# Optimization experiments

Measured on AMD Instinct MI355X. Metric: run time of the kernel, lower is better.

## Reference

```python
import jax, jax.numpy as jnp
import numpy as np

# ---- fixed structuring elements (buffers, not trainable) ----
N_SCALES = 4
BASE = 2.0
ZERO_SCALE = 1.0
PAD_VAL = 10000.0

_scales = ZERO_SCALE ** 2 * np.power(BASE, np.arange(N_SCALES)) ** 2  # t_k = 4^k
_widths = [4 * int(np.ceil(np.sqrt(s))) for s in _scales]             # 4,8,16,32
SES = [jnp.asarray([(1.0 / (4.0 * t)) * x ** 2 for x in range(-w, w + 1)],
                   dtype=jnp.float32)
       for t, w in zip(_scales, _widths)]  # SE lengths 9,17,33,65 (all odd)


def _pool1d(im, se, c, axis, is_max):
    """Weighted sliding max/min along `axis` (separable morphological op).
    out[p] = max_j padded[p+j] - c*se[j]  (dilation) or min_j padded[p+j] + c*se[j]."""
    n = se.shape[0]
    w = n // 2  # n is odd -> symmetric pad, matches torch pad1==pad2
    pad_val = -PAD_VAL if is_max else PAD_VAL
    cfg = [(0, 0)] * im.ndim
    cfg[axis] = (w, w)
    padded = jnp.pad(im, cfg, constant_values=pad_val)
    L = im.shape[axis]

    def take(j):
        return jax.lax.dynamic_slice_in_dim(padded, j, L, axis)

    win = jax.vmap(take)(jnp.arange(n))          # [n, B, C, H, W]
    se_b = se.reshape((n,) + (1,) * im.ndim)     # broadcast over image dims
    if is_max:
        return jnp.max(win - c * se_b, axis=0)
    return jnp.min(win + c * se_b, axis=0)


def _sep_dilation(im, se, c):
    tmp = _pool1d(im, se, c, axis=-1, is_max=True)   # horizontal
    return _pool1d(tmp, se, c, axis=-2, is_max=True)  # vertical


def _sep_erosion(im, se, c):
    tmp = _pool1d(im, se, c, axis=-1, is_max=False)
    return _pool1d(tmp, se, c, axis=-2, is_max=False)


def setup_inputs() -> dict:
    key = jax.random.key(0)
    k1, _ = jax.random.split(key)
    inputs = jax.random.normal(k1, (4, 8, 256, 256), dtype=jnp.float32)
    se_coef = jnp.float32(0.5)
    return {"inputs": inputs, "se_coef": se_coef}


def reference(inputs, se_coef):
    # closing = erosion(dilation(x)) per scale, stacked on new axis 2
    outs = [_sep_erosion(_sep_dilation(inputs, se, se_coef), se, se_coef)
            for se in SES]
    return jnp.stack(outs, axis=2)  # [B, C, n_scales, H, W]
```

## Files before the change

### kernel.cpp

```cpp
#include <hip/hip_runtime.h>


#define HH 256
#define WW 256
#define BC 32
#define NS 4
#define HW (HH * WW)
#define SLICE ((long)BC * HW)
#define LSTR 324

template <int W, bool IS_MAX>
__device__ __forceinline__ void hpass_lds(const float* __restrict__ lw, float cw,
                                          float acc[8])
{
    const float PAD = IS_MAX ? -1e30f : 1e30f;
#pragma unroll
    for (int pp = 0; pp < 8; ++pp) acc[pp] = PAD;
#pragma unroll
    for (int u = 0; u < (8 + 2 * W) / 4; ++u) {
        const float4 vv = *(const float4*)(lw + 4 * u);
        const float vs[4] = {vv.x, vv.y, vv.z, vv.w};
#pragma unroll
        for (int pp = 0; pp < 8; ++pp) {
#pragma unroll
            for (int e = 0; e < 4; ++e) {
                const int d = 4 * u + e - W - pp;
                if (d >= -W && d <= W) {
                    const float K = (float)(d * d);
                    const float cand = IS_MAX ? fmaf(cw, -K, vs[e])
                                              : fmaf(cw,  K, vs[e]);
                    acc[pp] = IS_MAX ? fmaxf(acc[pp], cand) : fminf(acc[pp], cand);
                }
            }
        }
    }
}

template <int W, bool IS_MAX, bool CLAMP>
__device__ __forceinline__ void vpass_core(const float* __restrict__ img, int x,
                                           int h0, float cw, float acc[8])
{
    const float PAD = IS_MAX ? -1e30f : 1e30f;
#pragma unroll
    for (int pp = 0; pp < 8; ++pp) acc[pp] = PAD;
#pragma unroll
    for (int ch = 0; ch < (8 + 2 * W) / 8; ++ch) {
        float v[8];
#pragma unroll
        for (int q = 0; q < 8; ++q) {
            const int h = h0 + ch * 8 + q - W;
            if (CLAMP) {
                const int hc = min(max(h, 0), HH - 1);
                const float tv = img[(long)hc * WW + x];
                v[q] = (h == hc) ? tv : PAD;
            } else {
                v[q] = img[(long)h * WW + x];
            }
        }
#pragma unroll
        for (int pp = 0; pp < 8; ++pp) {
#pragma unroll
            for (int q = 0; q < 8; ++q) {
                const int d = ch * 8 + q - W - pp;
                if (d >= -W && d <= W) {
                    const float K = (float)(d * d);
                    const float cand = IS_MAX ? fmaf(cw, -K, v[q])
                                              : fmaf(cw,  K, v[q]);
                    acc[pp] = IS_MAX ? fmaxf(acc[pp], cand) : fminf(acc[pp], cand);
                }
            }
        }
    }
}

template <int W, bool IS_MAX>
__device__ __forceinline__ void vh_impl(const float* __restrict__ img,
                                        float* __restrict__ op_base,
                                        int h0, float c, float* lbuf)
{
    const int x = threadIdx.x;
    const float cw = c * (4.0f / (float)(W * W));
    const float PAD = IS_MAX ? -1e30f : 1e30f;

    float vacc[8];
    if (h0 >= W && h0 + 8 + W <= HH)
        vpass_core<W, IS_MAX, false>(img, x, h0, cw, vacc);
    else
        vpass_core<W, IS_MAX, true >(img, x, h0, cw, vacc);

#pragma unroll
    for (int q = 0; q < 8; ++q) lbuf[q * LSTR + W + x] = vacc[q];
    if (x < W) {
#pragma unroll
        for (int q = 0; q < 8; ++q) {
            lbuf[q * LSTR + x] = PAD;
            lbuf[q * LSTR + W + 256 + x] = PAD;
        }
    }
    __syncthreads();

    const int r = threadIdx.x >> 5, t = threadIdx.x & 31;
    float acc[8];
    hpass_lds<W, IS_MAX>(lbuf + r * LSTR + 8 * t, cw, acc);
    float* op = op_base + (long)(h0 + r) * WW + 8 * t;
    *(float4*)(op)     = make_float4(acc[0], acc[1], acc[2], acc[3]);
    *(float4*)(op + 4) = make_float4(acc[4], acc[5], acc[6], acc[7]);
}

template <bool IS_MAX>
__global__ __launch_bounds__(256, 8) void k_vh(const float* __restrict__ in,
                                               float* __restrict__ out,
                                               const float* __restrict__ cptr,
                                               long in_ks, long in_zs,
                                               long out_ks, long out_zs,
                                               int kbase, int kbits,
                                               int zbase, int zbits)
{
    __shared__ float lbuf[8 * LSTR];
    const int bid = blockIdx.x;
    const int k = kbase + (bid & ((1 << kbits) - 1));
    const int rest = bid >> kbits;
    const int z = zbase + (rest & ((1 << zbits) - 1));
    const int y = rest >> zbits;
    const int h0 = y * 8;
    const float c = cptr[0];
    const float* ip = in + (long)k * in_ks + (long)z * in_zs;
    float* op = out + (long)k * out_ks + (long)z * out_zs;
    switch (k) {
        case 0: vh_impl<4,  IS_MAX>(ip, op, h0, c, lbuf); break;
        case 1: vh_impl<8,  IS_MAX>(ip, op, h0, c, lbuf); break;
        case 2: vh_impl<16, IS_MAX>(ip, op, h0, c, lbuf); break;
        case 3: vh_impl<32, IS_MAX>(ip, op, h0, c, lbuf); break;
    }
}

extern "C" void kernel_launch(void* const* d_in, const int* in_sizes, int n_in,
                              void* d_out, int out_size, void* d_ws, size_t ws_size,
                              hipStream_t stream)
{
    const float* x = (const float*)d_in[0];
    const float* c = (const float*)d_in[1];
    float* out = (float*)d_out;
    float* ws  = (float*)d_ws;

    dim3 b(256);
    const size_t slice_b = (size_t)SLICE * sizeof(float);
    if (ws_size >= (size_t)NS * slice_b) {
        dim3 g(NS * BC * (HH / 8));
        k_vh<true ><<<g, b, 0, stream>>>(x,  ws,  c, 0,     HW, SLICE, HW,
                                         0, 2, 0, 5);
        k_vh<false><<<g, b, 0, stream>>>(ws, out, c, SLICE, HW, HW, (long)NS * HW,
                                         0, 2, 0, 5);
    } else if (ws_size >= slice_b) {
        dim3 g(BC * (HH / 8));
        for (int k = 0; k < NS; ++k) {
            k_vh<true ><<<g, b, 0, stream>>>(x,  ws,  c, 0, HW, 0, HW,
                                             k, 0, 0, 5);
            k_vh<false><<<g, b, 0, stream>>>(ws, out, c, 0, HW, HW, (long)NS * HW,
                                             k, 0, 0, 5);
        }
    } else {
        dim3 g(HH / 8);
        for (int k = 0; k < NS; ++k)
            for (int z = 0; z < BC; ++z) {
                k_vh<true ><<<g, b, 0, stream>>>(x,  ws,  c, 0, HW, 0, 0,
                                                 k, 0, z, 0);
                k_vh<false><<<g, b, 0, stream>>>(ws, out, c, 0, 0, HW, (long)NS * HW,
                                                 k, 0, z, 0);
            }
    }
}
```

Measured before the change: 133.0 us.

## Balance block work across scales by looping multiple row tiles for small windows

Blocks now process a variable number of 8-row tiles: scale 3 (widest window) gets one tile per block, while smaller scales loop over 2, 4 or 8 tiles. The grid shrinks from 128 to 60 blocks per slice, so per-block work is more even across scales and fewer light blocks are launched. A trailing barrier is added so LDS can be reused between tiles. In exchange there is less total parallelism, with 1920 blocks, and the small-scale blocks run their tiles serially.

New measurement: 119.7 us (median of 2 runs). 10.0% less time.

```diff
diff --git a/kernel.cpp b/kernel.cpp
--- a/kernel.cpp
+++ b/kernel.cpp
@@ -74,12 +74,11 @@
 }
 
 template <int W, bool IS_MAX>
-__device__ __forceinline__ void vh_impl(const float* __restrict__ img,
+__device__ __forceinline__ void vh_tile(const float* __restrict__ img,
                                         float* __restrict__ op_base,
-                                        int h0, float c, float* lbuf)
+                                        int h0, float cw, float* lbuf)
 {
     const int x = threadIdx.x;
-    const float cw = c * (4.0f / (float)(W * W));
     const float PAD = IS_MAX ? -1e30f : 1e30f;
 
     float vacc[8];
@@ -105,6 +104,19 @@
     float* op = op_base + (long)(h0 + r) * WW + 8 * t;
     *(float4*)(op)     = make_float4(acc[0], acc[1], acc[2], acc[3]);
     *(float4*)(op + 4) = make_float4(acc[4], acc[5], acc[6], acc[7]);
+
+    __syncthreads();
+}
+
+template <int W, bool IS_MAX, int NT>
+__device__ __forceinline__ void run_tiles(const float* __restrict__ ip,
+                                          float* __restrict__ op,
+                                          int y0, float c, float* lbuf)
+{
+    const float cw = c * (4.0f / (float)(W * W));
+#pragma unroll 1
+    for (int i = 0; i < NT; ++i)
+        vh_tile<W, IS_MAX>(ip, op, (y0 + i) * 8, cw, lbuf);
 }
 
 template <bool IS_MAX>
@@ -113,24 +125,33 @@
                                                const float* __restrict__ cptr,
                                                long in_ks, long in_zs,
                                                long out_ks, long out_zs,
-                                               int kbase, int kbits,
-                                               int zbase, int zbits)
+                                               int kfix, int bpz, int zbase)
 {
     __shared__ float lbuf[8 * LSTR];
     const int bid = blockIdx.x;
-    const int k = kbase + (bid & ((1 << kbits) - 1));
-    const int rest = bid >> kbits;
-    const int z = zbase + (rest & ((1 << zbits) - 1));
-    const int y = rest >> zbits;
-    const int h0 = y * 8;
+    int k, y0, z;
+    if (kfix < 0) {
+        z = bid / 60;
+        const int r = bid - z * 60;
+        if (r < 32)      { k = 3; y0 = r; }
+        else if (r < 48) { k = 2; y0 = (r - 32) * 2; }
+        else if (r < 56) { k = 1; y0 = (r - 48) * 4; }
+        else             { k = 0; y0 = (r - 56) * 8; }
+    } else {
+        k = kfix;
+        const int zi = bid / bpz;
+        const int yi = bid - zi * bpz;
+        z = zbase + zi;
+        y0 = yi * (32 / bpz);
+    }
     const float c = cptr[0];
     const float* ip = in + (long)k * in_ks + (long)z * in_zs;
     float* op = out + (long)k * out_ks + (long)z * out_zs;
     switch (k) {
-        case 0: vh_impl<4,  IS_MAX>(ip, op, h0, c, lbuf); break;
-        case 1: vh_impl<8,  IS_MAX>(ip, op, h0, c, lbuf); break;
-        case 2: vh_impl<16, IS_MAX>(ip, op, h0, c, lbuf); break;
-        case 3: vh_impl<32, IS_MAX>(ip, op, h0, c, lbuf); break;
+        case 0: run_tiles<4,  IS_MAX, 8>(ip, op, y0, c, lbuf); break;
+        case 1: run_tiles<8,  IS_MAX, 4>(ip, op, y0, c, lbuf); break;
+        case 2: run_tiles<16, IS_MAX, 2>(ip, op, y0, c, lbuf); break;
+        case 3: run_tiles<32, IS_MAX, 1>(ip, op, y0, c, lbuf); break;
     }
 }
 
@@ -146,27 +167,30 @@
     dim3 b(256);
     const size_t slice_b = (size_t)SLICE * sizeof(float);
     if (ws_size >= (size_t)NS * slice_b) {
-        dim3 g(NS * BC * (HH / 8));
+        dim3 g(60 * BC);
         k_vh<true ><<<g, b, 0, stream>>>(x,  ws,  c, 0,     HW, SLICE, HW,
-                                         0, 2, 0, 5);
+                                         -1, 0, 0);
         k_vh<false><<<g, b, 0, stream>>>(ws, out, c, SLICE, HW, HW, (long)NS * HW,
-                                         0, 2, 0, 5);
+                                         -1, 0, 0);
     } else if (ws_size >= slice_b) {
-        dim3 g(BC * (HH / 8));
         for (int k = 0; k < NS; ++k) {
+            const int bpz = 4 << k;
+            dim3 g(bpz * BC);
             k_vh<true ><<<g, b, 0, stream>>>(x,  ws,  c, 0, HW, 0, HW,
-                                             k, 0, 0, 5);
+                                             k, bpz, 0);
             k_vh<false><<<g, b, 0, stream>>>(ws, out, c, 0, HW, HW, (long)NS * HW,
-                                             k, 0, 0, 5);
+                                             k, bpz, 0);
         }
     } else {
-        dim3 g(HH / 8);
-        for (int k = 0; k < NS; ++k)
+        for (int k = 0; k < NS; ++k) {
+            const int bpz = 4 << k;
+            dim3 g(bpz);
             for (int z = 0; z < BC; ++z) {
                 k_vh<true ><<<g, b, 0, stream>>>(x,  ws,  c, 0, HW, 0, 0,
-                                                 k, 0, z, 0);
+                                                 k, bpz, z);
                 k_vh<false><<<g, b, 0, stream>>>(ws, out, c, 0, 0, HW, (long)NS * HW,
-                                                 k, 0, z, 0);
+                                                 k, bpz, z);
             }
+        }
     }
 }
```
